# Kernel optimization log

Measured on AMD Instinct MI355X. Metric: run time of the kernel, lower is better.

The kernel has to match this reference:

```python
import jax, jax.numpy as jnp
import numpy as np

N_POINTS = 262144
L_LEVELS = 16
FEATS_PER_LEVEL = 2
BASE_RES = 8
FINEST_RES = 512
TABLE_SIZE = 2 ** 12  # log2_hashmap_size = 12
HIDDEN = 256
IN_FEATURES = 3
MLP_IN = L_LEVELS * FEATS_PER_LEVEL + IN_FEATURES - 2  # 33


def _level_params():
    b = np.exp((np.log(FINEST_RES) - np.log(BASE_RES)) / (L_LEVELS - 1))
    res = np.floor(BASE_RES * b ** np.arange(L_LEVELS)).astype(np.int64)
    hsize = np.minimum(res ** 2, TABLE_SIZE)  # per-level hashmap size
    return jnp.asarray(res, jnp.float32), jnp.asarray(hsize, jnp.uint32)


RES, HSIZE = _level_params()
PRIMES = jnp.array([1, 2654435761], dtype=jnp.uint32)  # instant-NGP spatial hash primes (2D)
CORNERS = jnp.array([[0, 0], [0, 1], [1, 0], [1, 1]], dtype=jnp.int32)  # [4,2]


def hash_encode(coords, tables):
    # coords: [N,2] in [0,1]; tables: [L, TABLE_SIZE, F]
    x = coords[None, :, :] * RES[:, None, None]            # [L,N,2] scaled per level
    xi = jnp.floor(x)
    xf = x - xi                                            # fractional part (grad flows to coords)
    inds = xi.astype(jnp.int32)[:, :, None, :] + CORNERS   # [L,N,4,2] corner integer coords
    # bilinear weights: offset 0 -> (1-xf), offset 1 -> xf
    w = jnp.prod(jnp.where(CORNERS == 0, 1.0 - xf[:, :, None, :], xf[:, :, None, :]), axis=-1)  # [L,N,4]
    u = inds.astype(jnp.uint32) * PRIMES                   # [L,N,4,2]
    h = (u[..., 0] ^ u[..., 1]) % HSIZE[:, None, None]     # [L,N,4] hashed table index
    feats = jax.vmap(lambda t, i: t[i])(tables, h)         # [L,N,4,F] gather per level
    out = jnp.einsum('lncf,lnc->lnf', feats, w)            # [L,N,F] bilinear interp
    return jnp.moveaxis(out, 0, 1).reshape(coords.shape[0], -1)  # [N, L*F], level-major per point


def reference(x, tables, W0, b0, W1, b1, W2, b2, W3, b3, W4, b4):
    h = hash_encode(x[:, :2], tables)                      # [N, 32]
    h = jnp.concatenate([h, x[:, 2:]], axis=-1)            # [N, 33]
    h = jax.nn.relu(h @ W0 + b0)
    h = jax.nn.relu(h @ W1 + b1)
    h = jax.nn.relu(h @ W2 + b2)
    h = jax.nn.relu(h @ W3 + b3)
    return h @ W4 + b4                                     # [N, 1]


def setup_inputs() -> dict:
    key = jax.random.key(0)
    ks = jax.random.split(key, 12)

    def lin(kw, fan_in, fan_out):
        s = 1.0 / np.sqrt(fan_in)
        return jax.random.normal(kw, (fan_in, fan_out), jnp.float32) * s

    return {
        'x': jax.random.uniform(ks[0], (N_POINTS, IN_FEATURES), jnp.float32),
        'tables': jax.random.normal(ks[1], (L_LEVELS, TABLE_SIZE, FEATS_PER_LEVEL), jnp.float32) * 1e-2,
        'W0': lin(ks[2], MLP_IN, HIDDEN), 'b0': jnp.zeros((HIDDEN,), jnp.float32),
        'W1': lin(ks[3], HIDDEN, HIDDEN), 'b1': jnp.zeros((HIDDEN,), jnp.float32),
        'W2': lin(ks[4], HIDDEN, HIDDEN), 'b2': jnp.zeros((HIDDEN,), jnp.float32),
        'W3': lin(ks[5], HIDDEN, HIDDEN), 'b3': jnp.zeros((HIDDEN,), jnp.float32),
        'W4': lin(ks[6], HIDDEN, 1),      'b4': jnp.zeros((1,), jnp.float32),
    }
```

## Files before the change

### kernel.cpp

```cpp
#include <hip/hip_runtime.h>
#include <math.h>


typedef __bf16 bf16x8 __attribute__((ext_vector_type(8)));
typedef float  f32x4  __attribute__((ext_vector_type(4)));
typedef unsigned int u32x4 __attribute__((ext_vector_type(4)));
typedef unsigned int u32x2 __attribute__((ext_vector_type(2)));

struct LevelParams { float res[16]; unsigned int hsize[16]; };

static constexpr int MTILE = 64;
static constexpr int LDA   = 264;
static constexpr int ACT_ELEMS = MTILE * LDA;
static constexpr int UNITS_L0 = 32;
static constexpr int UB_L0 = 0, UB_L1 = 32, UB_L2 = 160, UB_L3 = 288;
static constexpr int UNITS_TOTAL = 416;

__device__ __forceinline__ unsigned short f32_to_bf16_rne(float f) {
  unsigned u = __float_as_uint(f);
  unsigned r = (u + 0x7fffu + ((u >> 16) & 1u)) >> 16;
  return (unsigned short)r;
}
__device__ __forceinline__ float bf16_bits_to_f32(unsigned u16bits) {
  return __uint_as_float(u16bits << 16);
}

__global__ void prep_pack(const float* __restrict__ W0, const float* __restrict__ W1,
                          const float* __restrict__ W2, const float* __restrict__ W3,
                          unsigned short* __restrict__ pack) {
  int b = blockIdx.x;
  int lane = threadIdx.x;
  const float* W; int K; int r;
  if (b < UNITS_L0) { W = W0; K = 33; r = b; }
  else {
    int b2 = b - UNITS_L0; int ly = b2 >> 7; r = b2 & 127;
    W = (ly == 0) ? W1 : (ly == 1) ? W2 : W3; K = 256;
  }
  int s = r >> 4, ct = r & 15;
  int col   = (ct << 4) + (lane & 15);
  int kbase = (s << 5) + ((lane >> 4) << 3);
  unsigned short* dst = pack + (size_t)b * 1024;
#pragma unroll
  for (int e = 0; e < 8; ++e) {
    int k = kbase + e;
    float v = (k < K) ? W[k * 256 + col] : 0.0f;
    unsigned u = __float_as_uint(v);
    unsigned short h = (unsigned short)(u >> 16);
    float hf = bf16_bits_to_f32(u >> 16);
    unsigned short lo = f32_to_bf16_rne(v - hf);
    dst[lane * 8 + e]       = h;
    dst[512 + lane * 8 + e] = lo;
  }
}

__device__ __forceinline__ void run_layer(unsigned short* ahi, unsigned short* alo,
                                          const unsigned short* __restrict__ pack,
                                          int unitbase, int S,
                                          const float* __restrict__ bias,
                                          int wc, int lm, int lg, int lane) {
  f32x4 acc[4][2];
#pragma unroll
  for (int i = 0; i < 4; ++i)
#pragma unroll
    for (int j = 0; j < 2; ++j) acc[i][j] = (f32x4)0.0f;

  for (int s = 0; s < S; ++s) {
    bf16x8 w_h[2], w_l[2], a_h[4], a_l[4];
#pragma unroll
    for (int ct = 0; ct < 2; ++ct) {
      int unit = unitbase + (s << 4) + (wc << 1) + ct;
      const unsigned short* bp = pack + (size_t)unit * 1024 + (lane << 3);
      w_h[ct] = __builtin_bit_cast(bf16x8, *(const u32x4*)(bp));
      w_l[ct] = __builtin_bit_cast(bf16x8, *(const u32x4*)(bp + 512));
    }
#pragma unroll
    for (int pt = 0; pt < 4; ++pt) {
      int off = ((pt << 4) + lm) * LDA + (s << 5) + (lg << 3);
      a_h[pt] = __builtin_bit_cast(bf16x8, *(const u32x4*)(ahi + off));
      a_l[pt] = __builtin_bit_cast(bf16x8, *(const u32x4*)(alo + off));
    }
#pragma unroll
    for (int pt = 0; pt < 4; ++pt)
#pragma unroll
      for (int ct = 0; ct < 2; ++ct) {
        acc[pt][ct] = __builtin_amdgcn_mfma_f32_16x16x32_bf16(w_h[ct], a_h[pt], acc[pt][ct], 0, 0, 0);
        acc[pt][ct] = __builtin_amdgcn_mfma_f32_16x16x32_bf16(w_l[ct], a_h[pt], acc[pt][ct], 0, 0, 0);
        acc[pt][ct] = __builtin_amdgcn_mfma_f32_16x16x32_bf16(w_h[ct], a_l[pt], acc[pt][ct], 0, 0, 0);
      }
  }
  __syncthreads();
#pragma unroll
  for (int pt = 0; pt < 4; ++pt)
#pragma unroll
    for (int ct = 0; ct < 2; ++ct) {
      int colbase = (((wc << 1) + ct) << 4) + (lg << 2);
      float4 bv = *(const float4*)(bias + colbase);
      int base = ((pt << 4) + lm) * LDA + colbase;
      float v0 = fmaxf(acc[pt][ct][0] + bv.x, 0.0f);
      float v1 = fmaxf(acc[pt][ct][1] + bv.y, 0.0f);
      float v2 = fmaxf(acc[pt][ct][2] + bv.z, 0.0f);
      float v3 = fmaxf(acc[pt][ct][3] + bv.w, 0.0f);
      unsigned u0 = __float_as_uint(v0), u1 = __float_as_uint(v1);
      unsigned u2 = __float_as_uint(v2), u3 = __float_as_uint(v3);
      u32x2 hw = { (u0 >> 16) | (u1 & 0xffff0000u),
                   (u2 >> 16) | (u3 & 0xffff0000u) };
      float l0 = v0 - bf16_bits_to_f32(u0 >> 16);
      float l1 = v1 - bf16_bits_to_f32(u1 >> 16);
      float l2 = v2 - bf16_bits_to_f32(u2 >> 16);
      float l3 = v3 - bf16_bits_to_f32(u3 >> 16);
      u32x2 lw = { (unsigned)f32_to_bf16_rne(l0) | ((unsigned)f32_to_bf16_rne(l1) << 16),
                   (unsigned)f32_to_bf16_rne(l2) | ((unsigned)f32_to_bf16_rne(l3) << 16) };
      *(u32x2*)(ahi + base) = hw;
      *(u32x2*)(alo + base) = lw;
    }
  __syncthreads();
}

__global__ __launch_bounds__(512, 4) void inr_main(
    const float* __restrict__ x, const float* __restrict__ tables,
    const float* __restrict__ b0, const float* __restrict__ b1,
    const float* __restrict__ b2, const float* __restrict__ b3,
    const float* __restrict__ W4, const float* __restrict__ b4,
    const unsigned short* __restrict__ pack, float* __restrict__ out,
    LevelParams P) {
  extern __shared__ char smem[];
  unsigned short* ahi = (unsigned short*)smem;
  unsigned short* alo = ahi + ACT_ELEMS;

  const int tid = threadIdx.x;

  {
    int pl = tid >> 3, q = tid & 7;
    size_t p = (size_t)blockIdx.x * MTILE + pl;
    float x0 = x[3 * p + 0], x1 = x[3 * p + 1], x2 = x[3 * p + 2];
    float feat[4];
#pragma unroll
    for (int j = 0; j < 2; ++j) {
      int l = (q << 1) + j;
      float rf = P.res[l];
      unsigned hs = P.hsize[l];
      float xs0 = x0 * rf, xs1 = x1 * rf;
      float fl0 = floorf(xs0), fl1 = floorf(xs1);
      float f0 = xs0 - fl0, f1 = xs1 - fl1;
      int i0 = (int)fl0, i1 = (int)fl1;
      unsigned ua0 = (unsigned)i0, ua1 = (unsigned)(i0 + 1);
      unsigned vb0 = (unsigned)i1 * 2654435761u;
      unsigned vb1 = (unsigned)(i1 + 1) * 2654435761u;
      const float* tl = tables + ((size_t)l << 13);
      float g0 = 1.0f - f0, g1 = 1.0f - f1;
      float acc0 = 0.0f, acc1 = 0.0f;
      unsigned e0 = ua0 ^ vb0, e1 = ua0 ^ vb1, e2 = ua1 ^ vb0, e3 = ua1 ^ vb1;
      unsigned h0, h1, h2, h3;
      if (hs == 4096u) { h0 = e0 & 4095u; h1 = e1 & 4095u; h2 = e2 & 4095u; h3 = e3 & 4095u; }
      else             { h0 = e0 % hs;    h1 = e1 % hs;    h2 = e2 % hs;    h3 = e3 % hs; }
      { float w = g0 * g1; acc0 += w * tl[2*h0]; acc1 += w * tl[2*h0+1]; }
      { float w = g0 * f1; acc0 += w * tl[2*h1]; acc1 += w * tl[2*h1+1]; }
      { float w = f0 * g1; acc0 += w * tl[2*h2]; acc1 += w * tl[2*h2+1]; }
      { float w = f0 * f1; acc0 += w * tl[2*h3]; acc1 += w * tl[2*h3+1]; }
      feat[2*j] = acc0; feat[2*j+1] = acc1;
    }
    {
      int base = pl * LDA + (q << 2);
      unsigned u0 = __float_as_uint(feat[0]), u1 = __float_as_uint(feat[1]);
      unsigned u2 = __float_as_uint(feat[2]), u3 = __float_as_uint(feat[3]);
      u32x2 hw = { (u0 >> 16) | (u1 & 0xffff0000u), (u2 >> 16) | (u3 & 0xffff0000u) };
      float l0 = feat[0] - bf16_bits_to_f32(u0 >> 16);
      float l1 = feat[1] - bf16_bits_to_f32(u1 >> 16);
      float l2 = feat[2] - bf16_bits_to_f32(u2 >> 16);
      float l3 = feat[3] - bf16_bits_to_f32(u3 >> 16);
      u32x2 lw = { (unsigned)f32_to_bf16_rne(l0) | ((unsigned)f32_to_bf16_rne(l1) << 16),
                   (unsigned)f32_to_bf16_rne(l2) | ((unsigned)f32_to_bf16_rne(l3) << 16) };
      *(u32x2*)(ahi + base) = hw;
      *(u32x2*)(alo + base) = lw;
    }
    {
      int base = pl * LDA + 32 + (q << 2);
      if (q == 0) {
        unsigned u0 = __float_as_uint(x2);
        u32x2 hw = { u0 >> 16, 0u };
        float l0 = x2 - bf16_bits_to_f32(u0 >> 16);
        u32x2 lw = { (unsigned)f32_to_bf16_rne(l0), 0u };
        *(u32x2*)(ahi + base) = hw;
        *(u32x2*)(alo + base) = lw;
      } else {
        u32x2 z = { 0u, 0u };
        *(u32x2*)(ahi + base) = z;
        *(u32x2*)(alo + base) = z;
      }
    }
  }
  __syncthreads();

  const int lane = tid & 63;
  const int wc = tid >> 6;
  const int lm = lane & 15, lg = lane >> 4;

  run_layer(ahi, alo, pack, UB_L0, 2, b0, wc, lm, lg, lane);
  run_layer(ahi, alo, pack, UB_L1, 8, b1, wc, lm, lg, lane);
  run_layer(ahi, alo, pack, UB_L2, 8, b2, wc, lm, lg, lane);
  run_layer(ahi, alo, pack, UB_L3, 8, b3, wc, lm, lg, lane);

  {
    int pl = tid >> 3, q = tid & 7;
    const unsigned short* hrow = ahi + pl * LDA + (q << 5);
    const unsigned short* lrow = alo + pl * LDA + (q << 5);
    const float* w4p = W4 + (q << 5);
    float sum = 0.0f;
#pragma unroll
    for (int c = 0; c < 4; ++c) {
      u32x4 th = *(const u32x4*)(hrow + (c << 3));
      u32x4 tl = *(const u32x4*)(lrow + (c << 3));
      float4 wA = *(const float4*)(w4p + (c << 3));
      float4 wB = *(const float4*)(w4p + (c << 3) + 4);
#pragma unroll
      for (int e = 0; e < 4; ++e) {
        unsigned hu = th[e >> 1], lu = tl[e >> 1];
        unsigned sh = (e & 1) << 4;
        float v = bf16_bits_to_f32((hu >> sh) & 0xffffu) + bf16_bits_to_f32((lu >> sh) & 0xffffu);
        sum = fmaf(v, (&wA.x)[e], sum);
      }
#pragma unroll
      for (int e = 0; e < 4; ++e) {
        unsigned hu = th[2 + (e >> 1)], lu = tl[2 + (e >> 1)];
        unsigned sh = (e & 1) << 4;
        float v = bf16_bits_to_f32((hu >> sh) & 0xffffu) + bf16_bits_to_f32((lu >> sh) & 0xffffu);
        sum = fmaf(v, (&wB.x)[e], sum);
      }
    }
    sum += __shfl_xor(sum, 1);
    sum += __shfl_xor(sum, 2);
    sum += __shfl_xor(sum, 4);
    if (q == 0) out[(size_t)blockIdx.x * MTILE + pl] = sum + b4[0];
  }
}

extern "C" void kernel_launch(void* const* d_in, const int* in_sizes, int n_in,
                              void* d_out, int out_size, void* d_ws, size_t ws_size,
                              hipStream_t stream) {
  const float* x      = (const float*)d_in[0];
  const float* tables = (const float*)d_in[1];
  const float* W0 = (const float*)d_in[2];  const float* b0 = (const float*)d_in[3];
  const float* W1 = (const float*)d_in[4];  const float* b1 = (const float*)d_in[5];
  const float* W2 = (const float*)d_in[6];  const float* b2 = (const float*)d_in[7];
  const float* W3 = (const float*)d_in[8];  const float* b3 = (const float*)d_in[9];
  const float* W4 = (const float*)d_in[10]; const float* b4 = (const float*)d_in[11];
  unsigned short* pack = (unsigned short*)d_ws;
  float* out = (float*)d_out;

  LevelParams P;
  double bgrow = exp((log(512.0) - log(8.0)) / 15.0);
  for (int l = 0; l < 16; ++l) {
    double r = floor(8.0 * pow(bgrow, (double)l));
    P.res[l] = (float)r;
    double hsd = r * r;
    if (hsd > 4096.0) hsd = 4096.0;
    P.hsize[l] = (unsigned)hsd;
  }

  prep_pack<<<UNITS_TOTAL, 64, 0, stream>>>(W0, W1, W2, W3, pack);

  size_t smem_bytes = (size_t)ACT_ELEMS * 2 * 2;
  hipFuncSetAttribute(reinterpret_cast<const void*>(inr_main),
                      hipFuncAttributeMaxDynamicSharedMemorySize, (int)smem_bytes);

  int nblocks = out_size / MTILE;
  inr_main<<<nblocks, 512, smem_bytes, stream>>>(x, tables, b0, b1, b2, b3, W4, b4,
                                                 pack, out, P);
}
```

Measured before the change: 288.2 us.

## Replace hash modulo with magic-number division and fully unroll MFMA layer loops

Each thread now encodes one low-resolution level and one fixed 4096-size level, so no thread mixes modulo and mask paths. The modulo by a non-power-of-two table size is replaced by a 16-bit fold plus a host-precomputed multiply-high reciprocal. The layer loop becomes a template parameter so it fully unrolls, and the MFMAs are interleaved per A-tile. The hi/lo split of activations now truncates instead of rounding, which costs a little precision in the low bf16 half but saves ALU work.

Result: no change. 287.7 us (-0.2%).

```diff
diff --git a/kernel.cpp b/kernel.cpp
--- a/kernel.cpp
+++ b/kernel.cpp
@@ -7,7 +7,13 @@
 typedef unsigned int u32x4 __attribute__((ext_vector_type(4)));
 typedef unsigned int u32x2 __attribute__((ext_vector_type(2)));
 
-struct LevelParams { float res[16]; unsigned int hsize[16]; };
+struct LevelParams {
+  float res[16];
+  unsigned hsize[16];
+  unsigned M[8];
+  unsigned c16[8];
+  int      sh[8];
+};
 
 static constexpr int MTILE = 64;
 static constexpr int LDA   = 264;
@@ -23,6 +29,10 @@
 }
 __device__ __forceinline__ float bf16_bits_to_f32(unsigned u16bits) {
   return __uint_as_float(u16bits << 16);
+}
+
+__device__ __forceinline__ unsigned pack_hi(unsigned u0, unsigned u1) {
+  return (u0 >> 16) | (u1 & 0xffff0000u);
 }
 
 __global__ void prep_pack(const float* __restrict__ W0, const float* __restrict__ W1,
@@ -53,9 +63,11 @@
   }
 }
 
-__device__ __forceinline__ void run_layer(unsigned short* ahi, unsigned short* alo,
+template<int S>
+__device__ __forceinline__ void run_layer(unsigned short* __restrict__ ahi,
+                                          unsigned short* __restrict__ alo,
                                           const unsigned short* __restrict__ pack,
-                                          int unitbase, int S,
+                                          int unitbase,
                                           const float* __restrict__ bias,
                                           int wc, int lm, int lg, int lane) {
   f32x4 acc[4][2];
@@ -64,29 +76,28 @@
 #pragma unroll
     for (int j = 0; j < 2; ++j) acc[i][j] = (f32x4)0.0f;
 
+#pragma unroll
   for (int s = 0; s < S; ++s) {
-    bf16x8 w_h[2], w_l[2], a_h[4], a_l[4];
+    bf16x8 w_h[2], w_l[2];
 #pragma unroll
     for (int ct = 0; ct < 2; ++ct) {
-      int unit = unitbase + (s << 4) + (wc << 1) + ct;
-      const unsigned short* bp = pack + (size_t)unit * 1024 + (lane << 3);
+      const unsigned short* bp =
+          pack + (size_t)(unitbase + (s << 4) + (wc << 1) + ct) * 1024 + (lane << 3);
       w_h[ct] = __builtin_bit_cast(bf16x8, *(const u32x4*)(bp));
       w_l[ct] = __builtin_bit_cast(bf16x8, *(const u32x4*)(bp + 512));
     }
 #pragma unroll
     for (int pt = 0; pt < 4; ++pt) {
       int off = ((pt << 4) + lm) * LDA + (s << 5) + (lg << 3);
-      a_h[pt] = __builtin_bit_cast(bf16x8, *(const u32x4*)(ahi + off));
-      a_l[pt] = __builtin_bit_cast(bf16x8, *(const u32x4*)(alo + off));
-    }
-#pragma unroll
-    for (int pt = 0; pt < 4; ++pt)
-#pragma unroll
-      for (int ct = 0; ct < 2; ++ct) {
-        acc[pt][ct] = __builtin_amdgcn_mfma_f32_16x16x32_bf16(w_h[ct], a_h[pt], acc[pt][ct], 0, 0, 0);
-        acc[pt][ct] = __builtin_amdgcn_mfma_f32_16x16x32_bf16(w_l[ct], a_h[pt], acc[pt][ct], 0, 0, 0);
-        acc[pt][ct] = __builtin_amdgcn_mfma_f32_16x16x32_bf16(w_h[ct], a_l[pt], acc[pt][ct], 0, 0, 0);
-      }
+      bf16x8 a_h = __builtin_bit_cast(bf16x8, *(const u32x4*)(ahi + off));
+      bf16x8 a_l = __builtin_bit_cast(bf16x8, *(const u32x4*)(alo + off));
+      acc[pt][0] = __builtin_amdgcn_mfma_f32_16x16x32_bf16(w_h[0], a_h, acc[pt][0], 0, 0, 0);
+      acc[pt][1] = __builtin_amdgcn_mfma_f32_16x16x32_bf16(w_h[1], a_h, acc[pt][1], 0, 0, 0);
+      acc[pt][0] = __builtin_amdgcn_mfma_f32_16x16x32_bf16(w_l[0], a_h, acc[pt][0], 0, 0, 0);
+      acc[pt][1] = __builtin_amdgcn_mfma_f32_16x16x32_bf16(w_l[1], a_h, acc[pt][1], 0, 0, 0);
+      acc[pt][0] = __builtin_amdgcn_mfma_f32_16x16x32_bf16(w_h[0], a_l, acc[pt][0], 0, 0, 0);
+      acc[pt][1] = __builtin_amdgcn_mfma_f32_16x16x32_bf16(w_h[1], a_l, acc[pt][1], 0, 0, 0);
+    }
   }
   __syncthreads();
 #pragma unroll
@@ -102,14 +113,13 @@
       float v3 = fmaxf(acc[pt][ct][3] + bv.w, 0.0f);
       unsigned u0 = __float_as_uint(v0), u1 = __float_as_uint(v1);
       unsigned u2 = __float_as_uint(v2), u3 = __float_as_uint(v3);
-      u32x2 hw = { (u0 >> 16) | (u1 & 0xffff0000u),
-                   (u2 >> 16) | (u3 & 0xffff0000u) };
-      float l0 = v0 - bf16_bits_to_f32(u0 >> 16);
-      float l1 = v1 - bf16_bits_to_f32(u1 >> 16);
-      float l2 = v2 - bf16_bits_to_f32(u2 >> 16);
-      float l3 = v3 - bf16_bits_to_f32(u3 >> 16);
-      u32x2 lw = { (unsigned)f32_to_bf16_rne(l0) | ((unsigned)f32_to_bf16_rne(l1) << 16),
-                   (unsigned)f32_to_bf16_rne(l2) | ((unsigned)f32_to_bf16_rne(l3) << 16) };
+      u32x2 hw = { pack_hi(u0, u1), pack_hi(u2, u3) };
+      float l0 = v0 - __uint_as_float(u0 & 0xffff0000u);
+      float l1 = v1 - __uint_as_float(u1 & 0xffff0000u);
+      float l2 = v2 - __uint_as_float(u2 & 0xffff0000u);
+      float l3 = v3 - __uint_as_float(u3 & 0xffff0000u);
+      u32x2 lw = { pack_hi(__float_as_uint(l0), __float_as_uint(l1)),
+                   pack_hi(__float_as_uint(l2), __float_as_uint(l3)) };
       *(u32x2*)(ahi + base) = hw;
       *(u32x2*)(alo + base) = lw;
     }
@@ -133,12 +143,40 @@
     int pl = tid >> 3, q = tid & 7;
     size_t p = (size_t)blockIdx.x * MTILE + pl;
     float x0 = x[3 * p + 0], x1 = x[3 * p + 1], x2 = x[3 * p + 2];
-    float feat[4];
-#pragma unroll
-    for (int j = 0; j < 2; ++j) {
-      int l = (q << 1) + j;
+    float f_lo0, f_lo1, f_hi0, f_hi1;
+
+    {
+      float rf = P.res[q];
+      unsigned d = P.hsize[q], c = P.c16[q], M = P.M[q];
+      int sh = P.sh[q];
+      float xs0 = x0 * rf, xs1 = x1 * rf;
+      float fl0 = floorf(xs0), fl1 = floorf(xs1);
+      float f0 = xs0 - fl0, f1 = xs1 - fl1;
+      int i0 = (int)fl0, i1 = (int)fl1;
+      unsigned ua0 = (unsigned)i0, ua1 = (unsigned)(i0 + 1);
+      unsigned vb0 = (unsigned)i1 * 2654435761u;
+      unsigned vb1 = (unsigned)(i1 + 1) * 2654435761u;
+      const float* tl = tables + ((size_t)q << 13);
+      float g0 = 1.0f - f0, g1 = 1.0f - f1;
+      unsigned e0 = ua0 ^ vb0, e1 = ua0 ^ vb1, e2 = ua1 ^ vb0, e3 = ua1 ^ vb1;
+      unsigned n0 = (e0 >> 16) * c + (e0 & 0xffffu);
+      unsigned n1 = (e1 >> 16) * c + (e1 & 0xffffu);
+      unsigned n2 = (e2 >> 16) * c + (e2 & 0xffffu);
+      unsigned n3 = (e3 >> 16) * c + (e3 & 0xffffu);
+      unsigned h0 = n0 - (__umulhi(n0, M) >> sh) * d;
+      unsigned h1 = n1 - (__umulhi(n1, M) >> sh) * d;
+      unsigned h2 = n2 - (__umulhi(n2, M) >> sh) * d;
+      unsigned h3 = n3 - (__umulhi(n3, M) >> sh) * d;
+      float a0 = 0.0f, a1 = 0.0f;
+      { float w = g0 * g1; a0 += w * tl[2*h0]; a1 += w * tl[2*h0+1]; }
+      { float w = g0 * f1; a0 += w * tl[2*h1]; a1 += w * tl[2*h1+1]; }
+      { float w = f0 * g1; a0 += w * tl[2*h2]; a1 += w * tl[2*h2+1]; }
+      { float w = f0 * f1; a0 += w * tl[2*h3]; a1 += w * tl[2*h3+1]; }
+      f_lo0 = a0; f_lo1 = a1;
+    }
+    {
+      int l = q + 8;
       float rf = P.res[l];
-      unsigned hs = P.hsize[l];
       float xs0 = x0 * rf, xs1 = x1 * rf;
       float fl0 = floorf(xs0), fl1 = floorf(xs1);
       float f0 = xs0 - fl0, f1 = xs1 - fl1;
@@ -148,38 +186,35 @@
       unsigned vb1 = (unsigned)(i1 + 1) * 2654435761u;
       const float* tl = tables + ((size_t)l << 13);
       float g0 = 1.0f - f0, g1 = 1.0f - f1;
-      float acc0 = 0.0f, acc1 = 0.0f;
-      unsigned e0 = ua0 ^ vb0, e1 = ua0 ^ vb1, e2 = ua1 ^ vb0, e3 = ua1 ^ vb1;
-      unsigned h0, h1, h2, h3;
-      if (hs == 4096u) { h0 = e0 & 4095u; h1 = e1 & 4095u; h2 = e2 & 4095u; h3 = e3 & 4095u; }
-      else             { h0 = e0 % hs;    h1 = e1 % hs;    h2 = e2 % hs;    h3 = e3 % hs; }
-      { float w = g0 * g1; acc0 += w * tl[2*h0]; acc1 += w * tl[2*h0+1]; }
-      { float w = g0 * f1; acc0 += w * tl[2*h1]; acc1 += w * tl[2*h1+1]; }
-      { float w = f0 * g1; acc0 += w * tl[2*h2]; acc1 += w * tl[2*h2+1]; }
-      { float w = f0 * f1; acc0 += w * tl[2*h3]; acc1 += w * tl[2*h3+1]; }
-      feat[2*j] = acc0; feat[2*j+1] = acc1;
+      unsigned h0 = (ua0 ^ vb0) & 4095u, h1 = (ua0 ^ vb1) & 4095u;
+      unsigned h2 = (ua1 ^ vb0) & 4095u, h3 = (ua1 ^ vb1) & 4095u;
+      float a0 = 0.0f, a1 = 0.0f;
+      { float w = g0 * g1; a0 += w * tl[2*h0]; a1 += w * tl[2*h0+1]; }
+      { float w = g0 * f1; a0 += w * tl[2*h1]; a1 += w * tl[2*h1+1]; }
+      { float w = f0 * g1; a0 += w * tl[2*h2]; a1 += w * tl[2*h2+1]; }
+      { float w = f0 * f1; a0 += w * tl[2*h3]; a1 += w * tl[2*h3+1]; }
+      f_hi0 = a0; f_hi1 = a1;
     }
     {
-      int base = pl * LDA + (q << 2);
-      unsigned u0 = __float_as_uint(feat[0]), u1 = __float_as_uint(feat[1]);
-      unsigned u2 = __float_as_uint(feat[2]), u3 = __float_as_uint(feat[3]);
-      u32x2 hw = { (u0 >> 16) | (u1 & 0xffff0000u), (u2 >> 16) | (u3 & 0xffff0000u) };
-      float l0 = feat[0] - bf16_bits_to_f32(u0 >> 16);
-      float l1 = feat[1] - bf16_bits_to_f32(u1 >> 16);
-      float l2 = feat[2] - bf16_bits_to_f32(u2 >> 16);
-      float l3 = feat[3] - bf16_bits_to_f32(u3 >> 16);
-      u32x2 lw = { (unsigned)f32_to_bf16_rne(l0) | ((unsigned)f32_to_bf16_rne(l1) << 16),
-                   (unsigned)f32_to_bf16_rne(l2) | ((unsigned)f32_to_bf16_rne(l3) << 16) };
-      *(u32x2*)(ahi + base) = hw;
-      *(u32x2*)(alo + base) = lw;
+      int rowb = pl * LDA;
+      unsigned u0 = __float_as_uint(f_lo0), u1 = __float_as_uint(f_lo1);
+      unsigned u2 = __float_as_uint(f_hi0), u3 = __float_as_uint(f_hi1);
+      float l0 = f_lo0 - __uint_as_float(u0 & 0xffff0000u);
+      float l1 = f_lo1 - __uint_as_float(u1 & 0xffff0000u);
+      float l2 = f_hi0 - __uint_as_float(u2 & 0xffff0000u);
+      float l3 = f_hi1 - __uint_as_float(u3 & 0xffff0000u);
+      *(unsigned*)(ahi + rowb + 2*q)      = pack_hi(u0, u1);
+      *(unsigned*)(ahi + rowb + 16 + 2*q) = pack_hi(u2, u3);
+      *(unsigned*)(alo + rowb + 2*q)      = pack_hi(__float_as_uint(l0), __float_as_uint(l1));
+      *(unsigned*)(alo + rowb + 16 + 2*q) = pack_hi(__float_as_uint(l2), __float_as_uint(l3));
     }
     {
       int base = pl * LDA + 32 + (q << 2);
       if (q == 0) {
         unsigned u0 = __float_as_uint(x2);
+        float l0 = x2 - __uint_as_float(u0 & 0xffff0000u);
         u32x2 hw = { u0 >> 16, 0u };
-        float l0 = x2 - bf16_bits_to_f32(u0 >> 16);
-        u32x2 lw = { (unsigned)f32_to_bf16_rne(l0), 0u };
+        u32x2 lw = { __float_as_uint(l0) >> 16, 0u };
         *(u32x2*)(ahi + base) = hw;
         *(u32x2*)(alo + base) = lw;
       } else {
@@ -195,10 +230,10 @@
   const int wc = tid >> 6;
   const int lm = lane & 15, lg = lane >> 4;
 
-  run_layer(ahi, alo, pack, UB_L0, 2, b0, wc, lm, lg, lane);
-  run_layer(ahi, alo, pack, UB_L1, 8, b1, wc, lm, lg, lane);
-  run_layer(ahi, alo, pack, UB_L2, 8, b2, wc, lm, lg, lane);
-  run_layer(ahi, alo, pack, UB_L3, 8, b3, wc, lm, lg, lane);
+  run_layer<2>(ahi, alo, pack, UB_L0, b0, wc, lm, lg, lane);
+  run_layer<8>(ahi, alo, pack, UB_L1, b1, wc, lm, lg, lane);
+  run_layer<8>(ahi, alo, pack, UB_L2, b2, wc, lm, lg, lane);
+  run_layer<8>(ahi, alo, pack, UB_L3, b3, wc, lm, lg, lane);
 
   {
     int pl = tid >> 3, q = tid & 7;
@@ -213,18 +248,14 @@
       float4 wA = *(const float4*)(w4p + (c << 3));
       float4 wB = *(const float4*)(w4p + (c << 3) + 4);
 #pragma unroll
-      for (int e = 0; e < 4; ++e) {
-        unsigned hu = th[e >> 1], lu = tl[e >> 1];
-        unsigned sh = (e & 1) << 4;
-        float v = bf16_bits_to_f32((hu >> sh) & 0xffffu) + bf16_bits_to_f32((lu >> sh) & 0xffffu);
-        sum = fmaf(v, (&wA.x)[e], sum);
-      }
-#pragma unroll
-      for (int e = 0; e < 4; ++e) {
-        unsigned hu = th[2 + (e >> 1)], lu = tl[2 + (e >> 1)];
-        unsigned sh = (e & 1) << 4;
-        float v = bf16_bits_to_f32((hu >> sh) & 0xffffu) + bf16_bits_to_f32((lu >> sh) & 0xffffu);
-        sum = fmaf(v, (&wB.x)[e], sum);
+      for (int u = 0; u < 4; ++u) {
+        unsigned hu = th[u], lu = tl[u];
+        float v0 = __uint_as_float(hu << 16) + __uint_as_float(lu << 16);
+        float v1 = __uint_as_float(hu & 0xffff0000u) + __uint_as_float(lu & 0xffff0000u);
+        const float* wp = (u < 2) ? &wA.x : &wB.x;
+        int base = (u & 1) << 1;
+        sum = fmaf(v0, wp[base], sum);
+        sum = fmaf(v1, wp[base + 1], sum);
       }
     }
     sum += __shfl_xor(sum, 1);
@@ -256,6 +287,15 @@
     if (hsd > 4096.0) hsd = 4096.0;
     P.hsize[l] = (unsigned)hsd;
   }
+  for (int l = 0; l < 8; ++l) {
+    unsigned d = P.hsize[l];
+    P.c16[l] = 65536u % d;
+    unsigned long long nmax = 65535ULL * d;
+    int s = 0;
+    while (nmax * d >= (1ULL << (32 + s))) s++;
+    P.sh[l] = s;
+    P.M[l] = (unsigned)((1ULL << (32 + s)) / d + 1);
+  }
 
   prep_pack<<<UNITS_TOTAL, 64, 0, stream>>>(W0, W1, W2, W3, pack);
 
```
